# Kernel tuning notes

Measured on AMD Instinct MI355X. Metric: run time of the kernel, lower is better.

## Reference

```python
import jax, jax.numpy as jnp
import numpy as np

N, DIM, HEADS, E = 20000, 256, 4, 100000
C = DIM  # TransformerConv out_channels per head (concat=False averages heads)


def setup_inputs() -> dict:
    key = jax.random.key(0)
    ks = jax.random.split(key, 12)
    s = DIM ** -0.5
    w = lambda k, shape: jax.random.normal(k, shape, jnp.float32) * s
    z = lambda shape: jnp.zeros(shape, jnp.float32)
    return {
        "f_all": jax.random.normal(ks[0], (N, DIM), jnp.float32),
        "edge_index": jax.random.randint(ks[1], (2, E), 0, N),
        "W_gcn": w(ks[2], (DIM, DIM)), "b_gcn": z((DIM,)),
        "W_q": w(ks[3], (DIM, HEADS * C)), "b_q": z((HEADS * C,)),
        "W_k": w(ks[4], (DIM, HEADS * C)), "b_k": z((HEADS * C,)),
        "W_v": w(ks[5], (DIM, HEADS * C)), "b_v": z((HEADS * C,)),
        "W_skip": w(ks[6], (DIM, DIM)), "b_skip": z((DIM,)),
        "W_beta": w(ks[7], (3 * DIM, 1)),
        "W_cnn": w(ks[8], (DIM, DIM)), "b_cnn": z((DIM,)),
    }


def reference(f_all, edge_index, W_gcn, b_gcn, W_q, b_q, W_k, b_k, W_v, b_v,
              W_skip, b_skip, W_beta, W_cnn, b_cnn):
    src, dst = edge_index[0], edge_index[1]

    # --- GCNConv: add self loops, symmetric D^-1/2 (A+I) D^-1/2 normalization ---
    loop = jnp.arange(N)
    s2 = jnp.concatenate([src, loop])
    d2 = jnp.concatenate([dst, loop])
    deg = jax.ops.segment_sum(jnp.ones_like(d2, jnp.float32), d2, N)
    dinv = jnp.where(deg > 0, 1.0 / jnp.sqrt(deg), 0.0)
    norm = dinv[s2] * dinv[d2]                    # [E+N]
    h = f_all @ W_gcn                             # [N, DIM]
    x = jax.ops.segment_sum(h[s2] * norm[:, None], d2, N) + b_gcn
    x = jax.nn.relu(x)

    # --- TransformerConv(heads=H, concat=False, beta=True) ---
    q = (x @ W_q + b_q).reshape(N, HEADS, C)
    k = (x @ W_k + b_k).reshape(N, HEADS, C)
    v = (x @ W_v + b_v).reshape(N, HEADS, C)
    logits = jnp.einsum('ehc,ehc->eh', q[dst], k[src]) / np.float32(np.sqrt(C))
    m = jax.ops.segment_max(logits, dst, N)       # per-target max for stable softmax
    e = jnp.exp(logits - m[dst])
    denom = jax.ops.segment_sum(e, dst, N)
    alpha = e / jnp.maximum(denom[dst], 1e-16)    # [E, H]
    agg = jax.ops.segment_sum(v[src] * alpha[:, :, None], dst, N)  # [N, H, C]
    out = agg.mean(axis=1)                        # concat=False -> head average
    xr = x @ W_skip + b_skip                      # root/skip branch
    beta = jax.nn.sigmoid(jnp.concatenate([out, xr, out - xr], axis=-1) @ W_beta)
    tf = jax.nn.relu(beta * xr + (1.0 - beta) * out)  # [N, DIM]

    # --- Conv1d with kernel (dim,1) on [1,1,dim,N]: per-node linear, output [dim,N] ---
    conv = jnp.einsum('cd,nd->cn', W_cnn, tf) + b_cnn[:, None]  # [DIM, N]
    # torch does .view(1, n_mole, -1) on the [1,dim,1,N] conv output: raw reshape
    return conv.reshape(1, N, DIM)
```

## Files before the change

### kernel.cpp

```cpp
#include <hip/hip_runtime.h>
#include <math.h>

#define DIMC 256
#define NHEAD 4
#define CAP 64

typedef unsigned short bf16u;
typedef __attribute__((ext_vector_type(8))) short bf16x8;
typedef __attribute__((ext_vector_type(4))) float f32x4;

typedef __attribute__((address_space(1))) const unsigned char ga_u8;
typedef __attribute__((address_space(3))) unsigned char lds_u8;
__device__ __forceinline__ void gld_lds16(const void* g, void* l) {
    __builtin_amdgcn_global_load_lds((ga_u8*)g, (lds_u8*)l, 16, 0, 0);
}

__device__ __forceinline__ float bf2f(bf16u u) {
    union { float f; unsigned int i; } c; c.i = ((unsigned int)u) << 16; return c.f;
}
__device__ __forceinline__ bf16u f2bf(float f) {
    union { float f; unsigned int i; } c; c.f = f;
    unsigned int r = c.i + 0x7fffu + ((c.i >> 16) & 1u);
    return (bf16u)(r >> 16);
}
__device__ __forceinline__ float4 load_bf4(const bf16u* p) {
    ushort4 raw = *(const ushort4*)p;
    return make_float4(bf2f(raw.x), bf2f(raw.y), bf2f(raw.z), bf2f(raw.w));
}
__device__ __forceinline__ void store_bf4(bf16u* p, float4 v) {
    ushort4 raw;
    raw.x = f2bf(v.x); raw.y = f2bf(v.y); raw.z = f2bf(v.z); raw.w = f2bf(v.w);
    *(ushort4*)p = raw;
}
__device__ __forceinline__ void load_bf8(const bf16u* p, float* o) {
    bf16x8 raw = *(const bf16x8*)p;
#pragma unroll
    for (int i = 0; i < 8; ++i) {
        union { float f; unsigned int u; } c;
        c.u = ((unsigned int)(unsigned short)raw[i]) << 16;
        o[i] = c.f;
    }
}
__device__ __forceinline__ void store_bf8(bf16u* p, const float* v) {
    bf16x8 raw;
#pragma unroll
    for (int i = 0; i < 8; ++i) raw[i] = (short)f2bf(v[i]);
    *(bf16x8*)p = raw;
}


__global__ void fill_kernel(const int* __restrict__ src, const int* __restrict__ dst,
                            int* __restrict__ cursor, int* __restrict__ srcs, int E) {
    int e = blockIdx.x * 256 + threadIdx.x;
    if (e < E) {
        int d = dst[e];
        int pos = atomicAdd(&cursor[d], 1);
        if (pos < CAP) srcs[d * CAP + pos] = src[e];
    }
}


__global__ __launch_bounds__(256) void prep_kernel(const float* __restrict__ f_all, int n4_f,
                                                   const float* __restrict__ W_gcn,
                                                   const float* __restrict__ W_q,
                                                   const float* __restrict__ W_k,
                                                   const float* __restrict__ W_v,
                                                   const float* __restrict__ W_skip,
                                                   const float* __restrict__ W_cnn,
                                                   const float* __restrict__ b_q,
                                                   const float* __restrict__ b_k,
                                                   const float* __restrict__ b_v,
                                                   const float* __restrict__ b_skip,
                                                   bf16u* __restrict__ xbuf,
                                                   bf16u* __restrict__ WgcnT,
                                                   bf16u* __restrict__ WqkvsT,
                                                   bf16u* __restrict__ Wcnn_b,
                                                   float* __restrict__ bqkvs,
                                                   int* __restrict__ cursor, int N) {
    __shared__ float T[32][33];
    int b = blockIdx.x, t = threadIdx.x;
    int nf = (n4_f + 255) >> 8;
    int nz = (N + 255) >> 8;
    if (b < nf) {
        int i = b * 256 + t;
        if (i < n4_f) {
            float4 vv = *(const float4*)(f_all + (size_t)i * 4);
            store_bf4(xbuf + (size_t)i * 4, vv);
        }
        return;
    }
    b -= nf;
    if (b < 64) {
        int i = b * 256 + t;
        float4 vv = *(const float4*)(W_cnn + (size_t)i * 4);
        store_bf4(Wcnn_b + (size_t)i * 4, vv);
        return;
    }
    b -= 64;
    if (b < 13) {
        int i = b * 256 + t;
        if (i < 3328)
            bqkvs[i] = (i < 1024) ? b_q[i] : (i < 2048) ? b_k[i - 1024]
                     : (i < 3072) ? b_v[i - 2048] : b_skip[i - 3072];
        return;
    }
    b -= 13;
    if (b < nz) {
        int i = b * 256 + t;
        if (i < N) cursor[i] = 0;
        return;
    }
    b -= nz;
    const float* Wsrc; int N0, K0, ldw, ncol0; bf16u* out;
    if (b < 832) {
        N0 = (b % 104) * 32; K0 = (b / 104) * 32;
        if (N0 < 1024)      { Wsrc = W_q;    ncol0 = N0;        ldw = 1024; }
        else if (N0 < 2048) { Wsrc = W_k;    ncol0 = N0 - 1024; ldw = 1024; }
        else if (N0 < 3072) { Wsrc = W_v;    ncol0 = N0 - 2048; ldw = 1024; }
        else                { Wsrc = W_skip; ncol0 = N0 - 3072; ldw = 256;  }
        out = WqkvsT;
    } else {
        int bb = b - 832;
        N0 = (bb % 8) * 32; K0 = (bb / 8) * 32;
        Wsrc = W_gcn; ncol0 = N0; ldw = 256; out = WgcnT;
    }
    int tx = t & 31, ty = t >> 5;
#pragma unroll
    for (int i = 0; i < 4; ++i)
        T[ty + 8 * i][tx] = Wsrc[(size_t)(K0 + ty + 8 * i) * ldw + ncol0 + tx];
    __syncthreads();
#pragma unroll
    for (int i = 0; i < 4; ++i)
        out[(size_t)(N0 + ty + 8 * i) * 256 + K0 + tx] = f2bf(T[tx][ty + 8 * i]);
}


template <bool ROWBIAS>
__global__ __launch_bounds__(256) void gemm_tile(const bf16u* __restrict__ A,
                                                 const bf16u* __restrict__ BT,
                                                 const float* __restrict__ bias,
                                                 void* __restrict__ Cout,
                                                 int M, int Nc, int ldc) {
    __shared__ __align__(16) bf16u As[2][128][32];
    __shared__ __align__(16) bf16u Bs[2][128][32];
    int t = threadIdx.x;
    int w = t >> 6, lane = t & 63;
    int q = lane >> 4, r = lane & 15;
    int wm = (w & 1) * 64, wn = (w >> 1) * 64;
    int bm = blockIdx.y * 128, bn = blockIdx.x * 128;

    int srow = t >> 2, scol = (t & 3) * 8;
    int arow0 = bm + srow;      if (arow0 >= M)  arow0 = M - 1;
    int arow1 = bm + 64 + srow; if (arow1 >= M)  arow1 = M - 1;
    int brow0 = bn + srow;      if (brow0 >= Nc) brow0 = Nc - 1;
    int brow1 = bn + 64 + srow; if (brow1 >= Nc) brow1 = Nc - 1;
    const bf16u* a0 = A + (size_t)arow0 * DIMC + scol;
    const bf16u* a1 = A + (size_t)arow1 * DIMC + scol;
    const bf16u* b0 = BT + (size_t)brow0 * DIMC + scol;
    const bf16u* b1 = BT + (size_t)brow1 * DIMC + scol;

    char* As_base = (char*)&As[0][0][0] + w * 1024;
    char* Bs_base = (char*)&Bs[0][0][0] + w * 1024;

    f32x4 acc[4][4] = {};
    for (int g = 0; g < 4; ++g) {
        int k0 = g * 64;
        gld_lds16(a0 + k0, As_base);
        gld_lds16(a1 + k0, As_base + 4096);
        gld_lds16(b0 + k0, Bs_base);
        gld_lds16(b1 + k0, Bs_base + 4096);
        gld_lds16(a0 + k0 + 32, As_base + 8192);
        gld_lds16(a1 + k0 + 32, As_base + 8192 + 4096);
        gld_lds16(b0 + k0 + 32, Bs_base + 8192);
        gld_lds16(b1 + k0 + 32, Bs_base + 8192 + 4096);
        __syncthreads();
#pragma unroll
        for (int ks = 0; ks < 2; ++ks) {
            bf16x8 af[4], bfr[4];
#pragma unroll
            for (int i = 0; i < 4; ++i) af[i] = *(const bf16x8*)&As[ks][wm + i * 16 + r][q * 8];
#pragma unroll
            for (int j = 0; j < 4; ++j) bfr[j] = *(const bf16x8*)&Bs[ks][wn + j * 16 + r][q * 8];
#pragma unroll
            for (int i = 0; i < 4; ++i)
#pragma unroll
                for (int j = 0; j < 4; ++j)
                    acc[i][j] = __builtin_amdgcn_mfma_f32_16x16x32_bf16(af[i], bfr[j], acc[i][j], 0, 0, 0);
        }
        __syncthreads();
    }

    if (ROWBIAS) {
        float* C = (float*)Cout;
#pragma unroll
        for (int j = 0; j < 4; ++j) {
            int col = bn + wn + j * 16 + r;
            if (col >= Nc) continue;
#pragma unroll
            for (int i = 0; i < 4; ++i)
#pragma unroll
                for (int rg = 0; rg < 4; ++rg) {
                    int row = bm + wm + i * 16 + q * 4 + rg;
                    if (row < M)
                        __builtin_nontemporal_store(acc[i][j][rg] + bias[row],
                                                    &C[(size_t)row * ldc + col]);
                }
        }
    } else {
        __shared__ __align__(16) bf16u Cs[32][128];
        bf16u* C = (bf16u*)Cout;
        float cb4[4];
#pragma unroll
        for (int j = 0; j < 4; ++j) {
            int col = bn + wn + j * 16 + r;
            cb4[j] = bias ? bias[col] : 0.0f;
        }
        int rhalf = (w & 1) * 16;
        int colbase = (w >> 1) * 64;
        __syncthreads();
#pragma unroll
        for (int i = 0; i < 4; ++i) {
#pragma unroll
            for (int j = 0; j < 4; ++j)
#pragma unroll
                for (int rg = 0; rg < 4; ++rg)
                    Cs[rhalf + q * 4 + rg][colbase + j * 16 + r] = f2bf(acc[i][j][rg] + cb4[j]);
            __syncthreads();
#pragma unroll
            for (int cpass = 0; cpass < 2; ++cpass) {
                int chunk = cpass * 256 + t;
                int sr = chunk >> 4;
                int c16 = chunk & 15;
                int grow = bm + (sr < 16 ? i * 16 + sr : 64 + i * 16 + (sr - 16));
                if (grow < M)
                    __builtin_nontemporal_store(*(const bf16x8*)&Cs[sr][c16 * 8],
                                                (bf16x8*)&C[(size_t)grow * ldc + bn + c16 * 8]);
            }
            __syncthreads();
        }
    }
}


__global__ __launch_bounds__(256) void gcn_agg_kernel(const bf16u* __restrict__ h,
                                                      const int* __restrict__ cursor,
                                                      const int* __restrict__ srcs,
                                                      const float* __restrict__ b_gcn,
                                                      bf16u* __restrict__ x, int N) {
    int n = blockIdx.x * 8 + (threadIdx.x >> 5);
    if (n >= N) return;
    int lane = threadIdx.x & 31;
    int cb = lane * 8;
    int cnt = cursor[n]; if (cnt > CAP) cnt = CAP;
    float dn = rsqrtf((float)(cnt + 1));
    float hn[8];
    load_bf8(h + (size_t)n * DIMC + cb, hn);
    int base = n * CAP;
    float acc[8] = {};
    int i = 0;
    for (; i + 4 <= cnt; i += 4) {
        int4 s4 = *(const int4*)(srcs + base + i);
        float d0 = rsqrtf((float)(cursor[s4.x] + 1));
        float d1 = rsqrtf((float)(cursor[s4.y] + 1));
        float d2 = rsqrtf((float)(cursor[s4.z] + 1));
        float d3 = rsqrtf((float)(cursor[s4.w] + 1));
        float h0[8], h1[8], h2[8], h3[8];
        load_bf8(h + (size_t)s4.x * DIMC + cb, h0);
        load_bf8(h + (size_t)s4.y * DIMC + cb, h1);
        load_bf8(h + (size_t)s4.z * DIMC + cb, h2);
        load_bf8(h + (size_t)s4.w * DIMC + cb, h3);
#pragma unroll
        for (int j = 0; j < 8; ++j)
            acc[j] += h0[j] * d0 + h1[j] * d1 + h2[j] * d2 + h3[j] * d3;
    }
    for (; i < cnt; ++i) {
        int s = srcs[base + i];
        float ds = rsqrtf((float)(cursor[s] + 1));
        float hv[8];
        load_bf8(h + (size_t)s * DIMC + cb, hv);
#pragma unroll
        for (int j = 0; j < 8; ++j) acc[j] += hv[j] * ds;
    }
    float4 bg0 = *(const float4*)(b_gcn + cb);
    float4 bg1 = *(const float4*)(b_gcn + cb + 4);
    float bg[8] = {bg0.x, bg0.y, bg0.z, bg0.w, bg1.x, bg1.y, bg1.z, bg1.w};
    float dnn = dn * dn;
    float o[8];
#pragma unroll
    for (int j = 0; j < 8; ++j) o[j] = fmaxf(dn * acc[j] + hn[j] * dnn + bg[j], 0.f);
    store_bf8(x + (size_t)n * DIMC + cb, o);
}


__global__ __launch_bounds__(256) void transformer_kernel(const bf16u* __restrict__ qkv,
                                                          int stride,
                                                          const float* __restrict__ W_beta,
                                                          const int* __restrict__ cursor,
                                                          const int* __restrict__ srcs,
                                                          bf16u* __restrict__ tf, int N) {
    int n = blockIdx.x * 4 + (threadIdx.x >> 6);
    if (n >= N) return;
    int lane = threadIdx.x & 63;
    int hq = lane >> 4;
    int r = lane & 15;
    int c0 = hq * DIMC + r * 16;
    const float scale = 0.0625f;

    const bf16u* row_n = qkv + (size_t)n * stride;
    float qv[16];
    load_bf8(row_n + c0, qv);
    load_bf8(row_n + c0 + 8, qv + 8);
#pragma unroll
    for (int j = 0; j < 16; ++j) qv[j] *= scale;

    int cnt = cursor[n]; if (cnt > CAP) cnt = CAP;
    int base = n * CAP;
    float m = -INFINITY, denom = 0.f;
    float acc[16];
#pragma unroll
    for (int j = 0; j < 16; ++j) acc[j] = 0.f;

    const bf16u* kbase = qkv + 1024 + c0;
    const bf16u* vbase = qkv + 2048 + c0;

    int i = 0;
    for (; i + 2 <= cnt; i += 2) {
        int2 ss = *(const int2*)(srcs + base + i);
        const bf16u* k0p = kbase + (size_t)ss.x * stride;
        const bf16u* k1p = kbase + (size_t)ss.y * stride;
        const bf16u* v0p = vbase + (size_t)ss.x * stride;
        const bf16u* v1p = vbase + (size_t)ss.y * stride;
        float k0[16], k1[16], v0[16], v1[16];
        load_bf8(k0p, k0); load_bf8(k0p + 8, k0 + 8);
        load_bf8(k1p, k1); load_bf8(k1p + 8, k1 + 8);
        load_bf8(v0p, v0); load_bf8(v0p + 8, v0 + 8);
        load_bf8(v1p, v1); load_bf8(v1p + 8, v1 + 8);
        float d0 = 0.f, d1 = 0.f;
#pragma unroll
        for (int j = 0; j < 16; ++j) { d0 += qv[j] * k0[j]; d1 += qv[j] * k1[j]; }
#pragma unroll
        for (int msk = 1; msk <= 8; msk <<= 1) {
            d0 += __shfl_xor(d0, msk, 64);
            d1 += __shfl_xor(d1, msk, 64);
        }
        float nm = fmaxf(m, fmaxf(d0, d1));
        float so = __expf(m - nm);
        float p0 = __expf(d0 - nm);
        float p1 = __expf(d1 - nm);
        denom = denom * so + p0 + p1;
#pragma unroll
        for (int j = 0; j < 16; ++j) acc[j] = acc[j] * so + p0 * v0[j] + p1 * v1[j];
        m = nm;
    }
    if (i < cnt) {
        int s = srcs[base + i];
        const bf16u* kp = kbase + (size_t)s * stride;
        const bf16u* vp = vbase + (size_t)s * stride;
        float kk[16], vv[16];
        load_bf8(kp, kk); load_bf8(kp + 8, kk + 8);
        load_bf8(vp, vv); load_bf8(vp + 8, vv + 8);
        float d = 0.f;
#pragma unroll
        for (int j = 0; j < 16; ++j) d += qv[j] * kk[j];
#pragma unroll
        for (int msk = 1; msk <= 8; msk <<= 1) d += __shfl_xor(d, msk, 64);
        float nm = fmaxf(m, d);
        float so = __expf(m - nm);
        float p = __expf(d - nm);
        denom = denom * so + p;
#pragma unroll
        for (int j = 0; j < 16; ++j) acc[j] = acc[j] * so + p * vv[j];
        m = nm;
    }

    float inv = 1.0f / fmaxf(denom, 1e-16f);
#pragma unroll
    for (int j = 0; j < 16; ++j) acc[j] *= inv;
#pragma unroll
    for (int j = 0; j < 16; ++j) {
        acc[j] += __shfl_xor(acc[j], 16, 64);
        acc[j] += __shfl_xor(acc[j], 32, 64);
        acc[j] *= 0.25f;
    }

    float xv[16];
    load_bf8(row_n + 3072 + r * 16, xv);
    load_bf8(row_n + 3072 + r * 16 + 8, xv + 8);
    float contrib = 0.f;
#pragma unroll
    for (int j4 = 0; j4 < 4; ++j4) {
        float4 w0 = *(const float4*)(W_beta + r * 16 + j4 * 4);
        float4 w1 = *(const float4*)(W_beta + 256 + r * 16 + j4 * 4);
        float4 w2 = *(const float4*)(W_beta + 512 + r * 16 + j4 * 4);
        int j = j4 * 4;
        contrib += acc[j + 0] * w0.x + xv[j + 0] * w1.x + (acc[j + 0] - xv[j + 0]) * w2.x;
        contrib += acc[j + 1] * w0.y + xv[j + 1] * w1.y + (acc[j + 1] - xv[j + 1]) * w2.y;
        contrib += acc[j + 2] * w0.z + xv[j + 2] * w1.z + (acc[j + 2] - xv[j + 2]) * w2.z;
        contrib += acc[j + 3] * w0.w + xv[j + 3] * w1.w + (acc[j + 3] - xv[j + 3]) * w2.w;
    }
#pragma unroll
    for (int msk = 1; msk <= 8; msk <<= 1) contrib += __shfl_xor(contrib, msk, 64);
    float beta = 1.0f / (1.0f + __expf(-contrib));
    float tv[16];
#pragma unroll
    for (int j = 0; j < 16; ++j) tv[j] = fmaxf(beta * xv[j] + (1.0f - beta) * acc[j], 0.f);
    if (hq == 0) {
        store_bf8(tf + (size_t)n * DIMC + r * 16, tv);
        store_bf8(tf + (size_t)n * DIMC + r * 16 + 8, tv + 8);
    }
}


static inline size_t align_up(size_t x) { return (x + 255) & ~(size_t)255; }

extern "C" void kernel_launch(void* const* d_in, const int* in_sizes, int n_in,
                              void* d_out, int out_size, void* d_ws, size_t ws_size,
                              hipStream_t stream) {
    const float* f_all  = (const float*)d_in[0];
    const int*   eidx   = (const int*)d_in[1];
    const float* W_gcn  = (const float*)d_in[2];
    const float* b_gcn  = (const float*)d_in[3];
    const float* W_q    = (const float*)d_in[4];
    const float* b_q    = (const float*)d_in[5];
    const float* W_k    = (const float*)d_in[6];
    const float* b_k    = (const float*)d_in[7];
    const float* W_v    = (const float*)d_in[8];
    const float* b_v    = (const float*)d_in[9];
    const float* W_skip = (const float*)d_in[10];
    const float* b_skip = (const float*)d_in[11];
    const float* W_beta = (const float*)d_in[12];
    const float* W_cnn  = (const float*)d_in[13];
    const float* b_cnn  = (const float*)d_in[14];

    const int N = in_sizes[0] / DIMC;
    const int E = in_sizes[1] / 2;
    const int* src = eidx;
    const int* dst = eidx + E;

    char* p = (char*)d_ws;
    auto alloc = [&](size_t bytes) { char* r = p; p += align_up(bytes); return r; };
    int*   cursor  = (int*)alloc((size_t)N * 4);
    int*   srcs    = (int*)alloc((size_t)N * CAP * 4);
    bf16u* WgcnT   = (bf16u*)alloc(256 * 256 * 2);
    bf16u* WqkvsT  = (bf16u*)alloc((size_t)3328 * 256 * 2);
    float* bqkvs   = (float*)alloc(3328 * 4);
    bf16u* Wcnn_b  = (bf16u*)alloc(256 * 256 * 2);
    bf16u* xbuf    = (bf16u*)alloc((size_t)N * DIMC * 2);
    bf16u* h       = (bf16u*)alloc((size_t)N * DIMC * 2);
    bf16u* qkvs    = (bf16u*)alloc((size_t)N * 3328 * 2);

    int n4_f = N * DIMC / 4;
    int nf = (n4_f + 255) >> 8;
    int nz = (N + 255) >> 8;
    prep_kernel<<<nf + 64 + 13 + nz + 832 + 64, 256, 0, stream>>>(
        f_all, n4_f, W_gcn, W_q, W_k, W_v, W_skip, W_cnn,
        b_q, b_k, b_v, b_skip, xbuf, WgcnT, WqkvsT, Wcnn_b, bqkvs, cursor, N);

    fill_kernel<<<(E + 255) / 256, 256, 0, stream>>>(src, dst, cursor, srcs, E);

    int mby = (N + 127) / 128;
    gemm_tile<false><<<dim3(2, mby), 256, 0, stream>>>(xbuf, WgcnT, nullptr, h, N, 256, 256);
    gcn_agg_kernel<<<(N + 7) / 8, 256, 0, stream>>>(h, cursor, srcs, b_gcn, xbuf, N);
    gemm_tile<false><<<dim3(26, mby), 256, 0, stream>>>(xbuf, WqkvsT, bqkvs, qkvs, N, 3328, 3328);
    transformer_kernel<<<(N + 3) / 4, 256, 0, stream>>>(qkvs, 3328, W_beta,
                                                        cursor, srcs, h, N);
    gemm_tile<true><<<dim3((N + 127) / 128, 2), 256, 0, stream>>>(Wcnn_b, h, b_cnn, (float*)d_out, 256, N, N);
}
```

Before: 266.2 us.

## Fold Wq·Wkᵀ into query projection and apply Wv after aggregation

Logits are rewritten as (x_dst·Wq·Wk_hᵀ)·x_src. Each node computes a per-head projected query y (plus skip) and dots it with the raw bf16 x of each source, which replaces the K and V gathers. Values are aggregated in x-space per head and multiplied by Wv in a separate GEMM with K=1024, with the averaged b_v added for nodes that have edges. The big QKV GEMM shrinks from 3328 to 1280 output columns and gather traffic drops. In exchange there are a small Wq·Wkᵀ GEMM, an extra GEMM and beta kernel, a Z intermediate buffer, and bf16 rounding changes.

```diff
diff --git a/kernel.cpp b/kernel.cpp
--- a/kernel.cpp
+++ b/kernel.cpp
@@ -60,23 +60,19 @@
 }
 
 
-__global__ __launch_bounds__(256) void prep_kernel(const float* __restrict__ f_all, int n4_f,
-                                                   const float* __restrict__ W_gcn,
-                                                   const float* __restrict__ W_q,
-                                                   const float* __restrict__ W_k,
-                                                   const float* __restrict__ W_v,
-                                                   const float* __restrict__ W_skip,
-                                                   const float* __restrict__ W_cnn,
-                                                   const float* __restrict__ b_q,
-                                                   const float* __restrict__ b_k,
-                                                   const float* __restrict__ b_v,
-                                                   const float* __restrict__ b_skip,
-                                                   bf16u* __restrict__ xbuf,
-                                                   bf16u* __restrict__ WgcnT,
-                                                   bf16u* __restrict__ WqkvsT,
-                                                   bf16u* __restrict__ Wcnn_b,
-                                                   float* __restrict__ bqkvs,
-                                                   int* __restrict__ cursor, int N) {
+__global__ __launch_bounds__(256) void prep_kernel(
+    const float* __restrict__ f_all, int n4_f,
+    const float* __restrict__ W_gcn, const float* __restrict__ W_q,
+    const float* __restrict__ W_k, const float* __restrict__ W_v,
+    const float* __restrict__ W_skip, const float* __restrict__ W_cnn,
+    const float* __restrict__ b_q, const float* __restrict__ b_v,
+    const float* __restrict__ b_skip,
+    bf16u* __restrict__ xbuf, bf16u* __restrict__ WgcnT,
+    bf16u* __restrict__ BTyp, bf16u* __restrict__ BT_vs,
+    bf16u* __restrict__ A_wq, bf16u* __restrict__ A_wk,
+    bf16u* __restrict__ Wcnn_b,
+    float* __restrict__ ybias, float* __restrict__ bvm,
+    int* __restrict__ cursor, int N) {
     __shared__ float T[32][33];
     int b = blockIdx.x, t = threadIdx.x;
     int nf = (n4_f + 255) >> 8;
@@ -97,41 +93,65 @@
         return;
     }
     b -= 64;
-    if (b < 13) {
-        int i = b * 256 + t;
-        if (i < 3328)
-            bqkvs[i] = (i < 1024) ? b_q[i] : (i < 2048) ? b_k[i - 1024]
-                     : (i < 3072) ? b_v[i - 2048] : b_skip[i - 3072];
+    if (b < 4) {
+        int h = b, j = t;
+        const float4* bq4 = (const float4*)(b_q + h * 256);
+        const float4* wk4 = (const float4*)(W_k + (size_t)j * 1024 + h * 256);
+        float acc = 0.f;
+        for (int u = 0; u < 64; ++u) {
+            float4 a = bq4[u], w = wk4[u];
+            acc += a.x * w.x + a.y * w.y + a.z * w.z + a.w * w.w;
+        }
+        ybias[h * 256 + j] = acc;
         return;
     }
-    b -= 13;
+    b -= 4;
+    if (b < 1) {
+        ybias[1024 + t] = b_skip[t];
+        bvm[t] = 0.25f * (b_v[t] + b_v[256 + t] + b_v[512 + t] + b_v[768 + t]);
+        return;
+    }
+    b -= 1;
     if (b < nz) {
         int i = b * 256 + t;
         if (i < N) cursor[i] = 0;
         return;
     }
     b -= nz;
-    const float* Wsrc; int N0, K0, ldw, ncol0; bf16u* out;
-    if (b < 832) {
-        N0 = (b % 104) * 32; K0 = (b / 104) * 32;
-        if (N0 < 1024)      { Wsrc = W_q;    ncol0 = N0;        ldw = 1024; }
-        else if (N0 < 2048) { Wsrc = W_k;    ncol0 = N0 - 1024; ldw = 1024; }
-        else if (N0 < 3072) { Wsrc = W_v;    ncol0 = N0 - 2048; ldw = 1024; }
-        else                { Wsrc = W_skip; ncol0 = N0 - 3072; ldw = 256;  }
-        out = WqkvsT;
+    if (b < 512) {
+        const float* W = (b < 256) ? W_q : W_k;
+        bf16u* out = (b < 256) ? A_wq : A_wk;
+        int i4 = (b & 255) * 256 + t;
+        int e = i4 * 4;
+        int g = e >> 8, t4 = e & 255;
+        float4 vv = *(const float4*)(W + (size_t)(g & 255) * 1024 + (g >> 8) * 256 + t4);
+        store_bf4(out + (size_t)e, vv);
+        return;
+    }
+    b -= 512;
+    const float* src; bf16u* dst;
+    int inld, inrow0, incol0, outld, outrow0, outcol0;
+    if (b < 64) {
+        int N0 = (b & 7) * 32, K0 = (b >> 3) * 32;
+        src = W_gcn; inld = 256; inrow0 = K0; incol0 = N0;
+        dst = WgcnT; outld = 256; outrow0 = N0; outcol0 = K0;
+    } else if (b < 128) {
+        int bb = b - 64; int N0 = (bb & 7) * 32, K0 = (bb >> 3) * 32;
+        src = W_skip; inld = 256; inrow0 = K0; incol0 = N0;
+        dst = BTyp;  outld = 256; outrow0 = 1024 + N0; outcol0 = K0;
     } else {
-        int bb = b - 832;
-        N0 = (bb % 8) * 32; K0 = (bb / 8) * 32;
-        Wsrc = W_gcn; ncol0 = N0; ldw = 256; out = WgcnT;
+        int bb = b - 128; int jt = bb & 7, ct = (bb >> 3) & 7, hh = bb >> 6;
+        src = W_v;  inld = 1024; inrow0 = ct * 32; incol0 = hh * 256 + jt * 32;
+        dst = BT_vs; outld = 1024; outrow0 = jt * 32; outcol0 = hh * 256 + ct * 32;
     }
     int tx = t & 31, ty = t >> 5;
 #pragma unroll
     for (int i = 0; i < 4; ++i)
-        T[ty + 8 * i][tx] = Wsrc[(size_t)(K0 + ty + 8 * i) * ldw + ncol0 + tx];
+        T[ty + 8 * i][tx] = src[(size_t)(inrow0 + ty + 8 * i) * inld + incol0 + tx];
     __syncthreads();
 #pragma unroll
     for (int i = 0; i < 4; ++i)
-        out[(size_t)(N0 + ty + 8 * i) * 256 + K0 + tx] = f2bf(T[tx][ty + 8 * i]);
+        dst[(size_t)(outrow0 + ty + 8 * i) * outld + outcol0 + tx] = f2bf(T[tx][ty + 8 * i]);
 }
 
 
@@ -140,9 +160,12 @@
                                                  const bf16u* __restrict__ BT,
                                                  const float* __restrict__ bias,
                                                  void* __restrict__ Cout,
-                                                 int M, int Nc, int ldc) {
+                                                 int M, int Nc, int ldc, int K,
+                                                 int zstrA, int zstrB, int zstrC) {
     __shared__ __align__(16) bf16u As[2][128][32];
     __shared__ __align__(16) bf16u Bs[2][128][32];
+    A += (size_t)blockIdx.z * zstrA;
+    BT += (size_t)blockIdx.z * zstrB;
     int t = threadIdx.x;
     int w = t >> 6, lane = t & 63;
     int q = lane >> 4, r = lane & 15;
@@ -154,16 +177,17 @@
     int arow1 = bm + 64 + srow; if (arow1 >= M)  arow1 = M - 1;
     int brow0 = bn + srow;      if (brow0 >= Nc) brow0 = Nc - 1;
     int brow1 = bn + 64 + srow; if (brow1 >= Nc) brow1 = Nc - 1;
-    const bf16u* a0 = A + (size_t)arow0 * DIMC + scol;
-    const bf16u* a1 = A + (size_t)arow1 * DIMC + scol;
-    const bf16u* b0 = BT + (size_t)brow0 * DIMC + scol;
-    const bf16u* b1 = BT + (size_t)brow1 * DIMC + scol;
+    const bf16u* a0 = A + (size_t)arow0 * K + scol;
+    const bf16u* a1 = A + (size_t)arow1 * K + scol;
+    const bf16u* b0 = BT + (size_t)brow0 * K + scol;
+    const bf16u* b1 = BT + (size_t)brow1 * K + scol;
 
     char* As_base = (char*)&As[0][0][0] + w * 1024;
     char* Bs_base = (char*)&Bs[0][0][0] + w * 1024;
 
     f32x4 acc[4][4] = {};
-    for (int g = 0; g < 4; ++g) {
+    int ngroups = K >> 6;
+    for (int g = 0; g < ngroups; ++g) {
         int k0 = g * 64;
         gld_lds16(a0 + k0, As_base);
         gld_lds16(a1 + k0, As_base + 4096);
@@ -191,7 +215,7 @@
     }
 
     if (ROWBIAS) {
-        float* C = (float*)Cout;
+        float* C = (float*)Cout + (size_t)blockIdx.z * zstrC;
 #pragma unroll
         for (int j = 0; j < 4; ++j) {
             int col = bn + wn + j * 16 + r;
@@ -208,7 +232,7 @@
         }
     } else {
         __shared__ __align__(16) bf16u Cs[32][128];
-        bf16u* C = (bf16u*)Cout;
+        bf16u* C = (bf16u*)Cout + (size_t)blockIdx.z * zstrC;
         float cb4[4];
 #pragma unroll
         for (int j = 0; j < 4; ++j) {
@@ -292,26 +316,24 @@
 }
 
 
-__global__ __launch_bounds__(256) void transformer_kernel(const bf16u* __restrict__ qkv,
-                                                          int stride,
-                                                          const float* __restrict__ W_beta,
-                                                          const int* __restrict__ cursor,
-                                                          const int* __restrict__ srcs,
-                                                          bf16u* __restrict__ tf, int N) {
+__global__ __launch_bounds__(256) void attn_kernel(const bf16u* __restrict__ Y, int ldy,
+                                                   const bf16u* __restrict__ x,
+                                                   const int* __restrict__ cursor,
+                                                   const int* __restrict__ srcs,
+                                                   bf16u* __restrict__ Z, int N) {
     int n = blockIdx.x * 4 + (threadIdx.x >> 6);
     if (n >= N) return;
     int lane = threadIdx.x & 63;
     int hq = lane >> 4;
     int r = lane & 15;
-    int c0 = hq * DIMC + r * 16;
     const float scale = 0.0625f;
 
-    const bf16u* row_n = qkv + (size_t)n * stride;
-    float qv[16];
-    load_bf8(row_n + c0, qv);
-    load_bf8(row_n + c0 + 8, qv + 8);
-#pragma unroll
-    for (int j = 0; j < 16; ++j) qv[j] *= scale;
+    float yv[16];
+    const bf16u* yrow = Y + (size_t)n * ldy + hq * DIMC + r * 16;
+    load_bf8(yrow, yv);
+    load_bf8(yrow + 8, yv + 8);
+#pragma unroll
+    for (int j = 0; j < 16; ++j) yv[j] *= scale;
 
     int cnt = cursor[n]; if (cnt > CAP) cnt = CAP;
     int base = n * CAP;
@@ -320,24 +342,17 @@
 #pragma unroll
     for (int j = 0; j < 16; ++j) acc[j] = 0.f;
 
-    const bf16u* kbase = qkv + 1024 + c0;
-    const bf16u* vbase = qkv + 2048 + c0;
-
     int i = 0;
     for (; i + 2 <= cnt; i += 2) {
         int2 ss = *(const int2*)(srcs + base + i);
-        const bf16u* k0p = kbase + (size_t)ss.x * stride;
-        const bf16u* k1p = kbase + (size_t)ss.y * stride;
-        const bf16u* v0p = vbase + (size_t)ss.x * stride;
-        const bf16u* v1p = vbase + (size_t)ss.y * stride;
-        float k0[16], k1[16], v0[16], v1[16];
-        load_bf8(k0p, k0); load_bf8(k0p + 8, k0 + 8);
-        load_bf8(k1p, k1); load_bf8(k1p + 8, k1 + 8);
-        load_bf8(v0p, v0); load_bf8(v0p + 8, v0 + 8);
-        load_bf8(v1p, v1); load_bf8(v1p + 8, v1 + 8);
+        const bf16u* x0p = x + (size_t)ss.x * DIMC + r * 16;
+        const bf16u* x1p = x + (size_t)ss.y * DIMC + r * 16;
+        float x0[16], x1[16];
+        load_bf8(x0p, x0); load_bf8(x0p + 8, x0 + 8);
+        load_bf8(x1p, x1); load_bf8(x1p + 8, x1 + 8);
         float d0 = 0.f, d1 = 0.f;
 #pragma unroll
-        for (int j = 0; j < 16; ++j) { d0 += qv[j] * k0[j]; d1 += qv[j] * k1[j]; }
+        for (int j = 0; j < 16; ++j) { d0 += yv[j] * x0[j]; d1 += yv[j] * x1[j]; }
 #pragma unroll
         for (int msk = 1; msk <= 8; msk <<= 1) {
             d0 += __shfl_xor(d0, msk, 64);
@@ -349,19 +364,17 @@
         float p1 = __expf(d1 - nm);
         denom = denom * so + p0 + p1;
 #pragma unroll
-        for (int j = 0; j < 16; ++j) acc[j] = acc[j] * so + p0 * v0[j] + p1 * v1[j];
+        for (int j = 0; j < 16; ++j) acc[j] = acc[j] * so + p0 * x0[j] + p1 * x1[j];
         m = nm;
     }
     if (i < cnt) {
         int s = srcs[base + i];
-        const bf16u* kp = kbase + (size_t)s * stride;
-        const bf16u* vp = vbase + (size_t)s * stride;
-        float kk[16], vv[16];
-        load_bf8(kp, kk); load_bf8(kp + 8, kk + 8);
-        load_bf8(vp, vv); load_bf8(vp + 8, vv + 8);
+        const bf16u* xp = x + (size_t)s * DIMC + r * 16;
+        float xs[16];
+        load_bf8(xp, xs); load_bf8(xp + 8, xs + 8);
         float d = 0.f;
 #pragma unroll
-        for (int j = 0; j < 16; ++j) d += qv[j] * kk[j];
+        for (int j = 0; j < 16; ++j) d += yv[j] * xs[j];
 #pragma unroll
         for (int msk = 1; msk <= 8; msk <<= 1) d += __shfl_xor(d, msk, 64);
         float nm = fmaxf(m, d);
@@ -369,45 +382,51 @@
         float p = __expf(d - nm);
         denom = denom * so + p;
 #pragma unroll
-        for (int j = 0; j < 16; ++j) acc[j] = acc[j] * so + p * vv[j];
+        for (int j = 0; j < 16; ++j) acc[j] = acc[j] * so + p * xs[j];
         m = nm;
     }
 
-    float inv = 1.0f / fmaxf(denom, 1e-16f);
-#pragma unroll
-    for (int j = 0; j < 16; ++j) acc[j] *= inv;
-#pragma unroll
-    for (int j = 0; j < 16; ++j) {
-        acc[j] += __shfl_xor(acc[j], 16, 64);
-        acc[j] += __shfl_xor(acc[j], 32, 64);
-        acc[j] *= 0.25f;
-    }
-
-    float xv[16];
-    load_bf8(row_n + 3072 + r * 16, xv);
-    load_bf8(row_n + 3072 + r * 16 + 8, xv + 8);
+    float inv = 0.25f / fmaxf(denom, 1e-16f);
+    float o[16];
+#pragma unroll
+    for (int j = 0; j < 16; ++j) o[j] = acc[j] * inv;
+    bf16u* zrow = Z + (size_t)n * 1024 + hq * DIMC + r * 16;
+    store_bf8(zrow, o);
+    store_bf8(zrow + 8, o + 8);
+}
+
+
+__global__ __launch_bounds__(256) void beta_kernel(const bf16u* __restrict__ outz,
+                                                   const bf16u* __restrict__ Yp, int ldy,
+                                                   const float* __restrict__ bvm,
+                                                   const float* __restrict__ W_beta,
+                                                   const int* __restrict__ cursor,
+                                                   bf16u* __restrict__ tf, int N) {
+    int n = blockIdx.x * 8 + (threadIdx.x >> 5);
+    if (n >= N) return;
+    int lane = threadIdx.x & 31;
+    int cb = lane * 8;
+    float ov[8], xr[8];
+    load_bf8(outz + (size_t)n * DIMC + cb, ov);
+    load_bf8(Yp + (size_t)n * ldy + 1024 + cb, xr);
+    float gate = (cursor[n] > 0) ? 1.f : 0.f;
+#pragma unroll
+    for (int j = 0; j < 8; ++j) ov[j] += gate * bvm[cb + j];
     float contrib = 0.f;
 #pragma unroll
-    for (int j4 = 0; j4 < 4; ++j4) {
-        float4 w0 = *(const float4*)(W_beta + r * 16 + j4 * 4);
-        float4 w1 = *(const float4*)(W_beta + 256 + r * 16 + j4 * 4);
-        float4 w2 = *(const float4*)(W_beta + 512 + r * 16 + j4 * 4);
-        int j = j4 * 4;
-        contrib += acc[j + 0] * w0.x + xv[j + 0] * w1.x + (acc[j + 0] - xv[j + 0]) * w2.x;
-        contrib += acc[j + 1] * w0.y + xv[j + 1] * w1.y + (acc[j + 1] - xv[j + 1]) * w2.y;
-        contrib += acc[j + 2] * w0.z + xv[j + 2] * w1.z + (acc[j + 2] - xv[j + 2]) * w2.z;
-        contrib += acc[j + 3] * w0.w + xv[j + 3] * w1.w + (acc[j + 3] - xv[j + 3]) * w2.w;
-    }
-#pragma unroll
-    for (int msk = 1; msk <= 8; msk <<= 1) contrib += __shfl_xor(contrib, msk, 64);
+    for (int j = 0; j < 8; ++j) {
+        float w1 = W_beta[cb + j];
+        float w2 = W_beta[256 + cb + j];
+        float w3 = W_beta[512 + cb + j];
+        contrib += ov[j] * w1 + xr[j] * w2 + (ov[j] - xr[j]) * w3;
+    }
+#pragma unroll
+    for (int msk = 1; msk <= 16; msk <<= 1) contrib += __shfl_xor(contrib, msk, 64);
     float beta = 1.0f / (1.0f + __expf(-contrib));
-    float tv[16];
-#pragma unroll
-    for (int j = 0; j < 16; ++j) tv[j] = fmaxf(beta * xv[j] + (1.0f - beta) * acc[j], 0.f);
-    if (hq == 0) {
-        store_bf8(tf + (size_t)n * DIMC + r * 16, tv);
-        store_bf8(tf + (size_t)n * DIMC + r * 16 + 8, tv + 8);
-    }
+    float tv[8];
+#pragma unroll
+    for (int j = 0; j < 8; ++j) tv[j] = fmaxf(beta * xr[j] + (1.0f - beta) * ov[j], 0.f);
+    store_bf8(tf + (size_t)n * DIMC + cb, tv);
 }
 
 
@@ -423,7 +442,6 @@
     const float* W_q    = (const float*)d_in[4];
     const float* b_q    = (const float*)d_in[5];
     const float* W_k    = (const float*)d_in[6];
-    const float* b_k    = (const float*)d_in[7];
     const float* W_v    = (const float*)d_in[8];
     const float* b_v    = (const float*)d_in[9];
     const float* W_skip = (const float*)d_in[10];
@@ -439,30 +457,45 @@
 
     char* p = (char*)d_ws;
     auto alloc = [&](size_t bytes) { char* r = p; p += align_up(bytes); return r; };
-    int*   cursor  = (int*)alloc((size_t)N * 4);
-    int*   srcs    = (int*)alloc((size_t)N * CAP * 4);
-    bf16u* WgcnT   = (bf16u*)alloc(256 * 256 * 2);
-    bf16u* WqkvsT  = (bf16u*)alloc((size_t)3328 * 256 * 2);
-    float* bqkvs   = (float*)alloc(3328 * 4);
-    bf16u* Wcnn_b  = (bf16u*)alloc(256 * 256 * 2);
-    bf16u* xbuf    = (bf16u*)alloc((size_t)N * DIMC * 2);
-    bf16u* h       = (bf16u*)alloc((size_t)N * DIMC * 2);
-    bf16u* qkvs    = (bf16u*)alloc((size_t)N * 3328 * 2);
+    int*   cursor = (int*)alloc((size_t)N * 4);
+    int*   srcs   = (int*)alloc((size_t)N * CAP * 4);
+    bf16u* WgcnT  = (bf16u*)alloc(256 * 256 * 2);
+    bf16u* BTyp   = (bf16u*)alloc((size_t)1280 * 256 * 2);
+    bf16u* BT_vs  = (bf16u*)alloc((size_t)256 * 1024 * 2);
+    bf16u* A_wq   = (bf16u*)alloc((size_t)1024 * 256 * 2);
+    bf16u* A_wk   = (bf16u*)alloc((size_t)1024 * 256 * 2);
+    bf16u* Wcnn_b = (bf16u*)alloc(256 * 256 * 2);
+    float* ybias  = (float*)alloc(1280 * 4);
+    float* bvm    = (float*)alloc(256 * 4);
+    bf16u* xbuf   = (bf16u*)alloc((size_t)N * DIMC * 2);
+    bf16u* h      = (bf16u*)alloc((size_t)N * DIMC * 2);
+    bf16u* Yp     = (bf16u*)alloc((size_t)N * 1280 * 2);
+    bf16u* Z      = (bf16u*)alloc((size_t)N * 1024 * 2);
+    bf16u* outz   = (bf16u*)alloc((size_t)N * DIMC * 2);
 
     int n4_f = N * DIMC / 4;
     int nf = (n4_f + 255) >> 8;
     int nz = (N + 255) >> 8;
-    prep_kernel<<<nf + 64 + 13 + nz + 832 + 64, 256, 0, stream>>>(
+    prep_kernel<<<nf + 64 + 4 + 1 + nz + 512 + 384, 256, 0, stream>>>(
         f_all, n4_f, W_gcn, W_q, W_k, W_v, W_skip, W_cnn,
-        b_q, b_k, b_v, b_skip, xbuf, WgcnT, WqkvsT, Wcnn_b, bqkvs, cursor, N);
+        b_q, b_v, b_skip, xbuf, WgcnT, BTyp, BT_vs, A_wq, A_wk, Wcnn_b,
+        ybias, bvm, cursor, N);
 
     fill_kernel<<<(E + 255) / 256, 256, 0, stream>>>(src, dst, cursor, srcs, E);
 
+    gemm_tile<false><<<dim3(2, 2, 4), 256, 0, stream>>>(
+        A_wk, A_wq, nullptr, BTyp, 256, 256, 256, 256, 65536, 65536, 65536);
+
     int mby = (N + 127) / 128;
-    gemm_tile<false><<<dim3(2, mby), 256, 0, stream>>>(xbuf, WgcnT, nullptr, h, N, 256, 256);
+    gemm_tile<false><<<dim3(2, mby), 256, 0, stream>>>(
+        xbuf, WgcnT, nullptr, h, N, 256, 256, 256, 0, 0, 0);
     gcn_agg_kernel<<<(N + 7) / 8, 256, 0, stream>>>(h, cursor, srcs, b_gcn, xbuf, N);
-    gemm_tile<false><<<dim3(26, mby), 256, 0, stream>>>(xbuf, WqkvsT, bqkvs, qkvs, N, 3328, 3328);
-    transformer_kernel<<<(N + 3) / 4, 256, 0, stream>>>(qkvs, 3328, W_beta,
-                                                        cursor, srcs, h, N);
-    gemm_tile<true><<<dim3((N + 127) / 128, 2), 256, 0, stream>>>(Wcnn_b, h, b_cnn, (float*)d_out, 256, N, N);
-}
+    gemm_tile<false><<<dim3(10, mby), 256, 0, stream>>>(
+        xbuf, BTyp, ybias, Yp, N, 1280, 1280, 256, 0, 0, 0);
+    attn_kernel<<<(N + 3) / 4, 256, 0, stream>>>(Yp, 1280, xbuf, cursor, srcs, Z, N);
+    gemm_tile<false><<<dim3(2, mby), 256, 0, stream>>>(
+        Z, BT_vs, nullptr, outz, N, 256, 256, 1024, 0, 0, 0);
+    beta_kernel<<<(N + 7) / 8, 256, 0, stream>>>(outz, Yp, 1280, bvm, W_beta, cursor, h, N);
+    gemm_tile<true><<<dim3((N + 127) / 128, 2), 256, 0, stream>>>(
+        Wcnn_b, h, b_cnn, (float*)d_out, 256, N, N, 256, 0, 0, 0);
+}
```

After: 253.7 us. 1.05x faster.
